# Performance work log

Hardware: AMD Instinct MI355X
Metric: run time of the kernel (lower is better)

The kernel has to match this reference:

```python
import jax, jax.numpy as jnp
import numpy as np

B, C, F, T = 4, 64, 64, 128
IC = 32  # inter_channels = C // 2
EPS = 1e-5  # BatchNorm eps


def _conv1x1(x, w, b=None):
    # x: (B, Cin, H, W), w: (Cout, Cin)
    y = jnp.einsum('bchw,oc->bohw', x, w)
    if b is not None:
        y = y + b[None, :, None, None]
    return y


def _maxpool2(x):
    b, c, h, w = x.shape
    return x.reshape(b, c, h // 2, 2, w // 2, 2).max(axis=(3, 5))


def _pos_score(fsz, tsz, h2_w):
    # positional encoding is (fpos, tpos) in [0,1]; the 2->1 conv head makes the
    # pos_delta contribution separable: score(n,m) = s(n) - s(m)
    fpos = jnp.linspace(0.0, 1.0, fsz)
    tpos = jnp.linspace(0.0, 1.0, tsz)
    return (h2_w[0] * fpos[:, None] + h2_w[1] * tpos[None, :]).reshape(-1)


def setup_inputs() -> dict:
    key = jax.random.key(0)
    ks = jax.random.split(key, 16)
    s = 0.05
    inp = {
        'x': jax.random.normal(ks[0], (B, C, F, T), dtype=jnp.float32),
        'psi_w': jax.random.normal(ks[1], (IC, C)) * s,
        'psi_b': jax.random.normal(ks[2], (IC,)) * s,
        'theta_w': jax.random.normal(ks[3], (IC, C)) * s,
        'theta_b': jax.random.normal(ks[4], (IC,)) * s,
        'phi_w': jax.random.normal(ks[5], (IC, C)) * s,
        'phi_b': jax.random.normal(ks[6], (IC,)) * s,
        'h0_w': jax.random.normal(ks[7], (IC,)) * s,
        'h1_w': jax.random.normal(ks[8], (IC,)) * s,
        'h2_w': jax.random.normal(ks[9], (2,)) * s,
        'W_w': jax.random.normal(ks[10], (C, IC + 1)) * s,
        'W_b': jax.random.normal(ks[11], (C,)) * s,
        'bn_gamma': jax.random.normal(ks[12], (C,)) * s + 1.0,
        'bn_beta': jax.random.normal(ks[13], (C,)) * s,
        'bn_mean': jax.random.normal(ks[14], (C,)) * s,
        'bn_var': jax.random.uniform(ks[15], (C,), minval=0.5, maxval=1.5),
    }
    return inp


def reference(x, psi_w, psi_b, theta_w, theta_b, phi_w, phi_b,
              h0_w, h1_w, h2_w, W_w, W_b, bn_gamma, bn_beta, bn_mean, bn_var):
    Bs, Cs, Fs, Ts = x.shape
    N = Fs * Ts
    M = (Fs // 2) * (Ts // 2)

    psi_x = _maxpool2(_conv1x1(x, psi_w, psi_b))      # (B, IC, F/2, T/2)
    theta_x = _conv1x1(x, theta_w, theta_b)           # (B, IC, F, T)
    phi_x = _maxpool2(_conv1x1(x, phi_w, phi_b))      # (B, IC, F/2, T/2)

    # additive attention scores: relu(head0(theta) + head1(phi) + head2(pos_delta))
    t_score = jnp.einsum('bcft,c->bft', theta_x, h0_w).reshape(Bs, N)   # (B, N)
    p_score = jnp.einsum('bcft,c->bft', phi_x, h1_w).reshape(Bs, M)     # (B, M)
    a = _pos_score(Fs, Ts, h2_w)             # (N,) query pos contribution
    bpos = _pos_score(Fs // 2, Ts // 2, h2_w)  # (M,) key pos contribution
    f = jax.nn.relu((t_score + a[None, :])[:, :, None]
                    + (p_score - bpos[None, :])[:, None, :])  # (B, N, M)

    f_div = f / jnp.asarray(M, f.dtype)
    psi_flat = psi_x.reshape(Bs, IC, M)
    y = jnp.einsum('bnm,bcm->bcn', f_div, psi_flat).reshape(Bs, IC, Fs, Ts)

    # r_structure_type='zero' -> structure feature is zeros (1 extra channel)
    structure = jnp.zeros((Bs, 1, Fs, Ts), dtype=y.dtype)
    y = jnp.concatenate([y, structure], axis=1)       # (B, IC+1, F, T)

    wy = _conv1x1(y, W_w, W_b)                        # (B, C, F, T)
    inv = bn_gamma / jnp.sqrt(bn_var + EPS)
    wy = wy * inv[None, :, None, None] + (bn_beta - bn_mean * inv)[None, :, None, None]
    return wy + x
```

## Files before the change

kernel.cpp:

```cpp
#include <hip/hip_runtime.h>

#define B_ 4
#define C_ 64
#define F_ 64
#define T_ 128
#define IC_ 32
#define N_ 8192
#define M_ 2048

#define OFF_U      0
#define OFF_PSI2   32768
#define OFF_V      294912
#define OFF_VS     303104
#define OFF_Q0     311296
#define OFF_Q1     835840
#define WS_FLOATS  1360384

__device__ __align__(16) float g_ws[WS_FLOATS];
__device__ int g_perm[B_ * M_];

__global__ __launch_bounds__(256) void k_front(
    const float* __restrict__ x,
    const float* __restrict__ psi_w, const float* __restrict__ psi_b,
    const float* __restrict__ theta_w, const float* __restrict__ theta_b,
    const float* __restrict__ phi_w, const float* __restrict__ phi_b,
    const float* __restrict__ h0_w, const float* __restrict__ h1_w,
    const float* __restrict__ h2_w)
{
    float* __restrict__ ws = g_ws;
    __shared__ __align__(16) float xs[64 * 64];
    __shared__ float pw[32 * 65];
    __shared__ float fw[32 * 65];
    __shared__ float wt_l[64];

    const int tid = threadIdx.x;
    const int bid = blockIdx.x;
    const int b = bid >> 7;
    const int rem = bid & 127;
    const int fh = rem >> 2;
    const int q = rem & 3;
    const int c0 = q * 32;

    for (int idx = tid; idx < 4096; idx += 256) {
        int c = idx >> 6, r2 = (idx >> 5) & 1, tl = idx & 31;
        xs[idx] = x[(((size_t)b * 64 + c) * 64 + (2 * fh + r2)) * 128 + c0 + tl];
    }
    for (int idx = tid; idx < 2048; idx += 256) {
        int o = idx >> 6, c = idx & 63;
        pw[o * 65 + c] = psi_w[idx];
        fw[o * 65 + c] = phi_w[idx];
    }
    if (tid < 64) {
        float acc = 0.f;
        for (int o2 = 0; o2 < 32; ++o2)
            acc += h0_w[o2] * theta_w[o2 * 64 + tid];
        wt_l[tid] = acc;
    }
    __syncthreads();

    const float h20 = h2_w[0], h21 = h2_w[1];

    {
        const int o = tid & 31, g = tid >> 5;
        const float pb = psi_b[o], fb = phi_b[o], h1 = h1_w[o];
        float sp[2][4] = {{0,0,0,0},{0,0,0,0}};
        float sf[2][4] = {{0,0,0,0},{0,0,0,0}};
        const int hc0 = g, hc1 = g + 8;
        for (int c = 0; c < 64; ++c) {
            const float pwv = pw[o * 65 + c];
            const float fwv = fw[o * 65 + c];
            const float2 xa0 = *(const float2*)&xs[c * 64 + 2 * hc0];
            const float2 xb0 = *(const float2*)&xs[c * 64 + 32 + 2 * hc0];
            const float2 xa1 = *(const float2*)&xs[c * 64 + 2 * hc1];
            const float2 xb1 = *(const float2*)&xs[c * 64 + 32 + 2 * hc1];
            sp[0][0] += pwv * xa0.x; sp[0][1] += pwv * xa0.y;
            sp[0][2] += pwv * xb0.x; sp[0][3] += pwv * xb0.y;
            sf[0][0] += fwv * xa0.x; sf[0][1] += fwv * xa0.y;
            sf[0][2] += fwv * xb0.x; sf[0][3] += fwv * xb0.y;
            sp[1][0] += pwv * xa1.x; sp[1][1] += pwv * xa1.y;
            sp[1][2] += pwv * xb1.x; sp[1][3] += pwv * xb1.y;
            sf[1][0] += fwv * xa1.x; sf[1][1] += fwv * xa1.y;
            sf[1][2] += fwv * xb1.x; sf[1][3] += fwv * xb1.y;
        }
#pragma unroll
        for (int h = 0; h < 2; ++h) {
            const int hc = h ? hc1 : hc0;
            const float psiv = fmaxf(fmaxf(sp[h][0], sp[h][1]), fmaxf(sp[h][2], sp[h][3])) + pb;
            const float phiv = fmaxf(fmaxf(sf[h][0], sf[h][1]), fmaxf(sf[h][2], sf[h][3])) + fb;
            const int m = fh * 64 + q * 16 + hc;
            ws[OFF_PSI2 + ((size_t)b * 2048 + m) * 32 + o] = psiv;
            float tv = h1 * phiv;
            for (int mask = 1; mask < 32; mask <<= 1)
                tv += __shfl_xor(tv, mask, 64);
            if (o == 0) {
                const float bpos = h20 * (fh * (1.0f / 31.0f))
                                 + h21 * ((q * 16 + hc) * (1.0f / 63.0f));
                ws[OFF_V + b * 2048 + m] = tv - bpos;
            }
        }
    }

    if (tid < 64) {
        const int r2 = tid >> 5, tl = tid & 31;
        float acc = 0.f;
        for (int c = 0; c < 64; ++c)
            acc += xs[c * 64 + r2 * 32 + tl] * wt_l[c];
        float tb_ = 0.f;
        for (int o2 = 0; o2 < 32; ++o2)
            tb_ += h0_w[o2] * theta_b[o2];
        const int f = 2 * fh + r2, tt = c0 + tl;
        const int n = f * 128 + tt;
        const float a = h20 * (f * (1.0f / 63.0f)) + h21 * (tt * (1.0f / 127.0f));
        ws[OFF_U + b * 8192 + n] = acc + tb_ + a;
    }
}

__global__ __launch_bounds__(256) void k_rank()
{
    float* __restrict__ ws = g_ws;
    __shared__ __align__(16) float vl[2048];
    __shared__ int part[256];
    const int tid = threadIdx.x;
    const int b = blockIdx.x >> 7, chunk = blockIdx.x & 127;
    const float* v = ws + OFF_V + b * 2048;
    for (int i = tid; i < 2048; i += 256) vl[i] = v[i];
    __syncthreads();

    const int ml = tid & 15, jq = tid >> 4;
    const int m = chunk * 16 + ml;
    const float vm = vl[m];
    int cnt = 0;
    const float4* v4 = (const float4*)vl;
    const int j0 = jq * 32;
    for (int j4 = j0; j4 < j0 + 32; ++j4) {
        const float4 vv = v4[j4];
        const int jb = j4 * 4;
        cnt += (vv.x > vm) || (vv.x == vm && (jb    ) < m);
        cnt += (vv.y > vm) || (vv.y == vm && (jb + 1) < m);
        cnt += (vv.z > vm) || (vv.z == vm && (jb + 2) < m);
        cnt += (vv.w > vm) || (vv.w == vm && (jb + 3) < m);
    }
    part[tid] = cnt;
    __syncthreads();
    if (tid < 16) {
        int r = 0;
#pragma unroll
        for (int j = 0; j < 16; ++j) r += part[j * 16 + tid];
        ws[OFF_VS + b * 2048 + r] = vl[chunk * 16 + tid];
        g_perm[b * 2048 + r] = chunk * 16 + tid;
    }
}

__global__ __launch_bounds__(512) void k_scan(
    const float* __restrict__ W_w)
{
    float* __restrict__ ws = g_ws;
    __shared__ float Wrow[32];
    __shared__ float a0[512], a1[512];
    const int tid = threadIdx.x;
    const int b = blockIdx.x >> 6, o = blockIdx.x & 63;
    if (tid < 32) Wrow[tid] = W_w[o * 33 + tid];
    __syncthreads();

    const int* perm = g_perm + b * 2048;
    const float* vs = ws + OFF_VS + b * 2048;
    const float* psi2 = ws + OFF_PSI2 + (size_t)b * 2048 * 32;

    float zl[4], vlv[4];
    float s0 = 0.f, s1 = 0.f;
    const int base = tid * 4;
#pragma unroll
    for (int qq = 0; qq < 4; ++qq) {
        const int i = base + qq;
        const int mp = perm[i];
        const float4* pr = (const float4*)(psi2 + (size_t)mp * 32);
        float z = 0.f;
#pragma unroll
        for (int w = 0; w < 8; ++w) {
            const float4 p4 = pr[w];
            z += Wrow[4 * w] * p4.x + Wrow[4 * w + 1] * p4.y
               + Wrow[4 * w + 2] * p4.z + Wrow[4 * w + 3] * p4.w;
        }
        const float vv = vs[i];
        zl[qq] = z; vlv[qq] = vv;
        s0 += z; s1 += vv * z;
    }
    a0[tid] = s0; a1[tid] = s1;
    __syncthreads();
    for (int off = 1; off < 512; off <<= 1) {
        const float t0_ = (tid >= off) ? a0[tid - off] : 0.f;
        const float t1_ = (tid >= off) ? a1[tid - off] : 0.f;
        __syncthreads();
        a0[tid] += t0_; a1[tid] += t1_;
        __syncthreads();
    }
    float r0 = a0[tid] - s0, r1 = a1[tid] - s1;
    float* Q0 = ws + OFF_Q0 + (size_t)b * 2049 * 64;
    float* Q1 = ws + OFF_Q1 + (size_t)b * 2049 * 64;
#pragma unroll
    for (int qq = 0; qq < 4; ++qq) {
        r0 += zl[qq]; r1 += vlv[qq] * zl[qq];
        Q0[(size_t)(base + qq + 1) * 64 + o] = r0;
        Q1[(size_t)(base + qq + 1) * 64 + o] = r1;
    }
    if (tid == 0) { Q0[o] = 0.f; Q1[o] = 0.f; }
}

__global__ __launch_bounds__(512) void k_out(
    const float* __restrict__ x,
    const float* __restrict__ W_b,
    const float* __restrict__ bn_g, const float* __restrict__ bn_b,
    const float* __restrict__ bn_m, const float* __restrict__ bn_v,
    float* __restrict__ out)
{
    const float* __restrict__ ws = g_ws;
    __shared__ float tileb[64 * 65];
    __shared__ int karr[64];
    __shared__ float uarr[64];

    const int tid = threadIdx.x;
    const int b = blockIdx.x >> 7, tile = blockIdx.x & 127;
    const int n0 = tile * 64;

    const float* vs = ws + OFF_VS + b * 2048;
    if (tid < 64) {
        const float u = ws[OFF_U + b * 8192 + n0 + tid];
        const float thr = -u;
        int lo = 0, hi = 2048;
        while (lo < hi) {
            const int mid = (lo + hi) >> 1;
            if (vs[mid] > thr) lo = mid + 1; else hi = mid;
        }
        karr[tid] = lo;
        uarr[tid] = u;
    }
    __syncthreads();

    const int lane = tid & 63, w = tid >> 6;
    const float inv = bn_g[lane] * __frsqrt_rn(bn_v[lane] + 1e-5f);
    const float sft = W_b[lane] * inv + bn_b[lane] - bn_m[lane] * inv;
    const float* Q0 = ws + OFF_Q0 + (size_t)b * 2049 * 64;
    const float* Q1 = ws + OFF_Q1 + (size_t)b * 2049 * 64;

    for (int nl = w; nl < 64; nl += 8) {
        const int k = karr[nl];
        const float u = uarr[nl];
        const float q0 = Q0[(size_t)k * 64 + lane];
        const float q1 = Q1[(size_t)k * 64 + lane];
        const float raw = (u * q0 + q1) * (1.0f / 2048.0f);
        tileb[lane * 65 + nl] = raw * inv + sft;
    }
    __syncthreads();

    for (int idx = tid; idx < 2048; idx += 512) {
        const int o = idx >> 5, j2 = idx & 31;
        const size_t gi = ((size_t)b * 64 + o) * 8192 + n0 + 2 * j2;
        const float2 xv = *(const float2*)&x[gi];
        float2 r;
        r.x = tileb[o * 65 + 2 * j2] + xv.x;
        r.y = tileb[o * 65 + 2 * j2 + 1] + xv.y;
        *(float2*)&out[gi] = r;
    }
}

extern "C" void kernel_launch(void* const* d_in, const int* in_sizes, int n_in,
                              void* d_out, int out_size, void* d_ws, size_t ws_size,
                              hipStream_t stream)
{
    (void)in_sizes; (void)n_in; (void)out_size; (void)d_ws; (void)ws_size;
    const float* x       = (const float*)d_in[0];
    const float* psi_w   = (const float*)d_in[1];
    const float* psi_b   = (const float*)d_in[2];
    const float* theta_w = (const float*)d_in[3];
    const float* theta_b = (const float*)d_in[4];
    const float* phi_w   = (const float*)d_in[5];
    const float* phi_b   = (const float*)d_in[6];
    const float* h0_w    = (const float*)d_in[7];
    const float* h1_w    = (const float*)d_in[8];
    const float* h2_w    = (const float*)d_in[9];
    const float* W_w     = (const float*)d_in[10];
    const float* W_b     = (const float*)d_in[11];
    const float* bn_g    = (const float*)d_in[12];
    const float* bn_b    = (const float*)d_in[13];
    const float* bn_m    = (const float*)d_in[14];
    const float* bn_v    = (const float*)d_in[15];
    float* out = (float*)d_out;

    k_front<<<dim3(512), dim3(256), 0, stream>>>(x, psi_w, psi_b, theta_w, theta_b,
                                                 phi_w, phi_b, h0_w, h1_w, h2_w);
    k_rank<<<dim3(512), dim3(256), 0, stream>>>();
    k_scan<<<dim3(256), dim3(512), 0, stream>>>(W_w);
    k_out<<<dim3(512), dim3(512), 0, stream>>>(x, W_b, bn_g, bn_b, bn_m, bn_v, out);
}
```

Measured before the change: 137.4 us.

## Vectorize loads, shuffle-based scan, LDS binary search, and retune block sizes

The front kernel now loads x with float4 and reads LDS as float4 with the column pairing remapped. The rank kernel interleaves its comparison chunks to cut LDS bank conflicts. The scan kernel drops to 256 threads with 8 elements each and replaces the barrier-heavy Hillis-Steele LDS scan with wavefront shuffle scans plus a per-wave total. The output kernel stages the sorted keys in LDS for the binary search and uses 256 threads. Together these aim to reduce memory transactions and synchronisation overhead, at the cost of lower parallelism in the scan and output kernels.

Result: faster. 128.5 us (-6.5%).

```diff
diff --git a/kernel.cpp b/kernel.cpp
--- a/kernel.cpp
+++ b/kernel.cpp
@@ -19,7 +19,7 @@
 __device__ __align__(16) float g_ws[WS_FLOATS];
 __device__ int g_perm[B_ * M_];
 
-__global__ __launch_bounds__(256) void k_front(
+__global__ __launch_bounds__(256) void k1(
     const float* __restrict__ x,
     const float* __restrict__ psi_w, const float* __restrict__ psi_b,
     const float* __restrict__ theta_w, const float* __restrict__ theta_b,
@@ -28,7 +28,7 @@
     const float* __restrict__ h2_w)
 {
     float* __restrict__ ws = g_ws;
-    __shared__ __align__(16) float xs[64 * 64];
+    __shared__ __align__(16) float xs[4096];
     __shared__ float pw[32 * 65];
     __shared__ float fw[32 * 65];
     __shared__ float wt_l[64];
@@ -41,12 +41,13 @@
     const int q = rem & 3;
     const int c0 = q * 32;
 
-    for (int idx = tid; idx < 4096; idx += 256) {
-        int c = idx >> 6, r2 = (idx >> 5) & 1, tl = idx & 31;
-        xs[idx] = x[(((size_t)b * 64 + c) * 64 + (2 * fh + r2)) * 128 + c0 + tl];
+    for (int idx = tid; idx < 1024; idx += 256) {
+        const int c = idx >> 4, r2 = (idx >> 3) & 1, t4 = idx & 7;
+        const float4 v = *(const float4*)&x[(((size_t)b * 64 + c) * 64 + (2 * fh + r2)) * 128 + c0 + 4 * t4];
+        *(float4*)&xs[c * 64 + r2 * 32 + 4 * t4] = v;
     }
     for (int idx = tid; idx < 2048; idx += 256) {
-        int o = idx >> 6, c = idx & 63;
+        const int o = idx >> 6, c = idx & 63;
         pw[o * 65 + c] = psi_w[idx];
         fw[o * 65 + c] = phi_w[idx];
     }
@@ -65,26 +66,23 @@
         const float pb = psi_b[o], fb = phi_b[o], h1 = h1_w[o];
         float sp[2][4] = {{0,0,0,0},{0,0,0,0}};
         float sf[2][4] = {{0,0,0,0},{0,0,0,0}};
-        const int hc0 = g, hc1 = g + 8;
         for (int c = 0; c < 64; ++c) {
             const float pwv = pw[o * 65 + c];
             const float fwv = fw[o * 65 + c];
-            const float2 xa0 = *(const float2*)&xs[c * 64 + 2 * hc0];
-            const float2 xb0 = *(const float2*)&xs[c * 64 + 32 + 2 * hc0];
-            const float2 xa1 = *(const float2*)&xs[c * 64 + 2 * hc1];
-            const float2 xb1 = *(const float2*)&xs[c * 64 + 32 + 2 * hc1];
-            sp[0][0] += pwv * xa0.x; sp[0][1] += pwv * xa0.y;
-            sp[0][2] += pwv * xb0.x; sp[0][3] += pwv * xb0.y;
-            sf[0][0] += fwv * xa0.x; sf[0][1] += fwv * xa0.y;
-            sf[0][2] += fwv * xb0.x; sf[0][3] += fwv * xb0.y;
-            sp[1][0] += pwv * xa1.x; sp[1][1] += pwv * xa1.y;
-            sp[1][2] += pwv * xb1.x; sp[1][3] += pwv * xb1.y;
-            sf[1][0] += fwv * xa1.x; sf[1][1] += fwv * xa1.y;
-            sf[1][2] += fwv * xb1.x; sf[1][3] += fwv * xb1.y;
+            const float4 r0v = *(const float4*)&xs[c * 64 + 4 * g];
+            const float4 r1v = *(const float4*)&xs[c * 64 + 32 + 4 * g];
+            sp[0][0] += pwv * r0v.x; sp[0][1] += pwv * r0v.y;
+            sp[0][2] += pwv * r1v.x; sp[0][3] += pwv * r1v.y;
+            sp[1][0] += pwv * r0v.z; sp[1][1] += pwv * r0v.w;
+            sp[1][2] += pwv * r1v.z; sp[1][3] += pwv * r1v.w;
+            sf[0][0] += fwv * r0v.x; sf[0][1] += fwv * r0v.y;
+            sf[0][2] += fwv * r1v.x; sf[0][3] += fwv * r1v.y;
+            sf[1][0] += fwv * r0v.z; sf[1][1] += fwv * r0v.w;
+            sf[1][2] += fwv * r1v.z; sf[1][3] += fwv * r1v.w;
         }
 #pragma unroll
         for (int h = 0; h < 2; ++h) {
-            const int hc = h ? hc1 : hc0;
+            const int hc = 2 * g + h;
             const float psiv = fmaxf(fmaxf(sp[h][0], sp[h][1]), fmaxf(sp[h][2], sp[h][3])) + pb;
             const float phiv = fmaxf(fmaxf(sf[h][0], sf[h][1]), fmaxf(sf[h][2], sf[h][3])) + fb;
             const int m = fh * 64 + q * 16 + hc;
@@ -115,7 +113,7 @@
     }
 }
 
-__global__ __launch_bounds__(256) void k_rank()
+__global__ __launch_bounds__(256) void k2()
 {
     float* __restrict__ ws = g_ws;
     __shared__ __align__(16) float vl[2048];
@@ -126,13 +124,15 @@
     for (int i = tid; i < 2048; i += 256) vl[i] = v[i];
     __syncthreads();
 
-    const int ml = tid & 15, jq = tid >> 4;
+    const int ml = tid >> 4;
+    const int jq = tid & 15;
     const int m = chunk * 16 + ml;
     const float vm = vl[m];
     int cnt = 0;
     const float4* v4 = (const float4*)vl;
-    const int j0 = jq * 32;
-    for (int j4 = j0; j4 < j0 + 32; ++j4) {
+#pragma unroll 4
+    for (int i = 0; i < 32; ++i) {
+        const int j4 = jq + 16 * i;
         const float4 vv = v4[j4];
         const int jb = j4 * 4;
         cnt += (vv.x > vm) || (vv.x == vm && (jb    ) < m);
@@ -145,18 +145,17 @@
     if (tid < 16) {
         int r = 0;
 #pragma unroll
-        for (int j = 0; j < 16; ++j) r += part[j * 16 + tid];
+        for (int j = 0; j < 16; ++j) r += part[tid * 16 + j];
         ws[OFF_VS + b * 2048 + r] = vl[chunk * 16 + tid];
         g_perm[b * 2048 + r] = chunk * 16 + tid;
     }
 }
 
-__global__ __launch_bounds__(512) void k_scan(
-    const float* __restrict__ W_w)
+__global__ __launch_bounds__(256) void k3(const float* __restrict__ W_w)
 {
     float* __restrict__ ws = g_ws;
     __shared__ float Wrow[32];
-    __shared__ float a0[512], a1[512];
+    __shared__ float wt0[4], wt1[4];
     const int tid = threadIdx.x;
     const int b = blockIdx.x >> 6, o = blockIdx.x & 63;
     if (tid < 32) Wrow[tid] = W_w[o * 33 + tid];
@@ -166,11 +165,11 @@
     const float* vs = ws + OFF_VS + b * 2048;
     const float* psi2 = ws + OFF_PSI2 + (size_t)b * 2048 * 32;
 
-    float zl[4], vlv[4];
+    float zl[8], vlv[8];
     float s0 = 0.f, s1 = 0.f;
-    const int base = tid * 4;
-#pragma unroll
-    for (int qq = 0; qq < 4; ++qq) {
+    const int base = tid * 8;
+#pragma unroll
+    for (int qq = 0; qq < 8; ++qq) {
         const int i = base + qq;
         const int mp = perm[i];
         const float4* pr = (const float4*)(psi2 + (size_t)mp * 32);
@@ -185,20 +184,25 @@
         zl[qq] = z; vlv[qq] = vv;
         s0 += z; s1 += vv * z;
     }
-    a0[tid] = s0; a1[tid] = s1;
-    __syncthreads();
-    for (int off = 1; off < 512; off <<= 1) {
-        const float t0_ = (tid >= off) ? a0[tid - off] : 0.f;
-        const float t1_ = (tid >= off) ? a1[tid - off] : 0.f;
-        __syncthreads();
-        a0[tid] += t0_; a1[tid] += t1_;
-        __syncthreads();
-    }
-    float r0 = a0[tid] - s0, r1 = a1[tid] - s1;
+
+    float w0 = s0, w1 = s1;
+    const int lane = tid & 63, wv = tid >> 6;
+#pragma unroll
+    for (int off = 1; off < 64; off <<= 1) {
+        const float t0_ = __shfl_up(w0, off, 64);
+        const float t1_ = __shfl_up(w1, off, 64);
+        if (lane >= off) { w0 += t0_; w1 += t1_; }
+    }
+    if (lane == 63) { wt0[wv] = w0; wt1[wv] = w1; }
+    __syncthreads();
+    float base0 = 0.f, base1 = 0.f;
+    for (int w = 0; w < wv; ++w) { base0 += wt0[w]; base1 += wt1[w]; }
+    float r0 = w0 + base0 - s0, r1 = w1 + base1 - s1;
+
     float* Q0 = ws + OFF_Q0 + (size_t)b * 2049 * 64;
     float* Q1 = ws + OFF_Q1 + (size_t)b * 2049 * 64;
 #pragma unroll
-    for (int qq = 0; qq < 4; ++qq) {
+    for (int qq = 0; qq < 8; ++qq) {
         r0 += zl[qq]; r1 += vlv[qq] * zl[qq];
         Q0[(size_t)(base + qq + 1) * 64 + o] = r0;
         Q1[(size_t)(base + qq + 1) * 64 + o] = r1;
@@ -206,7 +210,7 @@
     if (tid == 0) { Q0[o] = 0.f; Q1[o] = 0.f; }
 }
 
-__global__ __launch_bounds__(512) void k_out(
+__global__ __launch_bounds__(256) void k4(
     const float* __restrict__ x,
     const float* __restrict__ W_b,
     const float* __restrict__ bn_g, const float* __restrict__ bn_b,
@@ -214,6 +218,7 @@
     float* __restrict__ out)
 {
     const float* __restrict__ ws = g_ws;
+    __shared__ __align__(16) float vsl[2048];
     __shared__ float tileb[64 * 65];
     __shared__ int karr[64];
     __shared__ float uarr[64];
@@ -223,13 +228,16 @@
     const int n0 = tile * 64;
 
     const float* vs = ws + OFF_VS + b * 2048;
+    for (int i = tid; i < 2048; i += 256) vsl[i] = vs[i];
+    __syncthreads();
+
     if (tid < 64) {
         const float u = ws[OFF_U + b * 8192 + n0 + tid];
         const float thr = -u;
         int lo = 0, hi = 2048;
         while (lo < hi) {
             const int mid = (lo + hi) >> 1;
-            if (vs[mid] > thr) lo = mid + 1; else hi = mid;
+            if (vsl[mid] > thr) lo = mid + 1; else hi = mid;
         }
         karr[tid] = lo;
         uarr[tid] = u;
@@ -242,7 +250,7 @@
     const float* Q0 = ws + OFF_Q0 + (size_t)b * 2049 * 64;
     const float* Q1 = ws + OFF_Q1 + (size_t)b * 2049 * 64;
 
-    for (int nl = w; nl < 64; nl += 8) {
+    for (int nl = w; nl < 64; nl += 4) {
         const int k = karr[nl];
         const float u = uarr[nl];
         const float q0 = Q0[(size_t)k * 64 + lane];
@@ -252,7 +260,7 @@
     }
     __syncthreads();
 
-    for (int idx = tid; idx < 2048; idx += 512) {
+    for (int idx = tid; idx < 2048; idx += 256) {
         const int o = idx >> 5, j2 = idx & 31;
         const size_t gi = ((size_t)b * 64 + o) * 8192 + n0 + 2 * j2;
         const float2 xv = *(const float2*)&x[gi];
@@ -286,9 +294,9 @@
     const float* bn_v    = (const float*)d_in[15];
     float* out = (float*)d_out;
 
-    k_front<<<dim3(512), dim3(256), 0, stream>>>(x, psi_w, psi_b, theta_w, theta_b,
-                                                 phi_w, phi_b, h0_w, h1_w, h2_w);
-    k_rank<<<dim3(512), dim3(256), 0, stream>>>();
-    k_scan<<<dim3(256), dim3(512), 0, stream>>>(W_w);
-    k_out<<<dim3(512), dim3(512), 0, stream>>>(x, W_b, bn_g, bn_b, bn_m, bn_v, out);
-}
+    k1<<<dim3(512), dim3(256), 0, stream>>>(x, psi_w, psi_b, theta_w, theta_b,
+                                            phi_w, phi_b, h0_w, h1_w, h2_w);
+    k2<<<dim3(512), dim3(256), 0, stream>>>();
+    k3<<<dim3(256), dim3(256), 0, stream>>>(W_w);
+    k4<<<dim3(512), dim3(256), 0, stream>>>(x, W_b, bn_g, bn_b, bn_m, bn_v, out);
+}
```
